# Kernel optimization log

Hardware: AMD Instinct MI355X
Metric: run time of the kernel (lower is better)

Reference implementation:

```python
import jax, jax.numpy as jnp
import numpy as np

B = 131072
IN, H1, H2, OUT = 784, 128, 64, 10


def setup_inputs() -> dict:
    key = jax.random.key(0)
    ks = jax.random.split(key, 10)
    f16 = jnp.float16
    x = jax.random.normal(ks[0], (B, IN), dtype=f16)
    # int4 quantized weights: values in [-8, 7], stored as int32
    w1_q = jax.random.randint(ks[1], (H1, IN), -8, 8, dtype=jnp.int32)
    w2_q = jax.random.randint(ks[2], (H2, H1), -8, 8, dtype=jnp.int32)
    w3_q = jax.random.randint(ks[3], (OUT, H2), -8, 8, dtype=jnp.int32)
    # per-output-channel scales ~ kaiming-ish magnitude / 7 (int4 max)
    s1 = (jax.random.uniform(ks[4], (H1,), dtype=f16) * f16(0.02) + f16(0.005))
    s2 = (jax.random.uniform(ks[5], (H2,), dtype=f16) * f16(0.02) + f16(0.005))
    s3 = (jax.random.uniform(ks[6], (OUT,), dtype=f16) * f16(0.02) + f16(0.005))
    b1 = jax.random.normal(ks[7], (H1,), dtype=f16) * f16(0.01)
    b2 = jax.random.normal(ks[8], (H2,), dtype=f16) * f16(0.01)
    b3 = jax.random.normal(ks[9], (OUT,), dtype=f16) * f16(0.01)
    return {"x": x, "w1_q": w1_q, "s1": s1, "b1": b1,
            "w2_q": w2_q, "s2": s2, "b2": b2,
            "w3_q": w3_q, "s3": s3, "b3": b3}


def _qlinear(x, w_q, scale, bias):
    # W4A16: dequantize int4 weights with per-out-channel scale, fp16 GEMM + bias
    w = w_q.astype(jnp.float16) * scale[:, None]  # [out, in]
    return jnp.dot(x, w.T) + bias


def reference(x, w1_q, s1, b1, w2_q, s2, b2, w3_q, s3, b3):
    x = x.reshape(-1, IN)
    h = jax.nn.relu(_qlinear(x, w1_q, s1, b1))
    h = jax.nn.relu(_qlinear(h, w2_q, s2, b2))
    return _qlinear(h, w3_q, s3, b3)
```

## Files before the change

kernel.cpp:

```cpp
#include <hip/hip_runtime.h>
#include <hip/hip_bf16.h>

#define NROWS 131072
#define KIN   784
#define H1N   128
#define H2N   64
#define OUTN  10

#define W1P_DW    12800
#define W2C_ELEMS (16 * 64 * 8)
#define W3_ELEMS  (16 * 64)

typedef short s16x8 __attribute__((ext_vector_type(8)));
typedef float f32x4 __attribute__((ext_vector_type(4)));
typedef __hip_bfloat16 bf16;

static __device__ __forceinline__ short b2s(float f) {
    bf16 h = __float2bfloat16(f);
    return *reinterpret_cast<short*>(&h);
}
static __device__ __forceinline__ s16x8 cvt8(f32x4 a, f32x4 b) {
    s16x8 r;
    r[0] = b2s(a[0]); r[1] = b2s(a[1]); r[2] = b2s(a[2]); r[3] = b2s(a[3]);
    r[4] = b2s(b[0]); r[5] = b2s(b[1]); r[6] = b2s(b[2]); r[7] = b2s(b[3]);
    return r;
}
static __device__ __forceinline__ s16x8 unpack8(unsigned d) {
    s16x8 r;
#pragma unroll
    for (int j = 0; j < 8; ++j) {
        int v = ((int)(d << (28 - 4 * j))) >> 28;
        r[j] = b2s((float)v);
    }
    return r;
}
static __device__ __forceinline__ void gl2lds16(const void* g, char* l) {
    __builtin_amdgcn_global_load_lds(
        (const __attribute__((address_space(1))) void*)g,
        (__attribute__((address_space(3))) void*)l, 16, 0, 0);
}
static __device__ __forceinline__ void gl2lds4(const void* g, char* l) {
    __builtin_amdgcn_global_load_lds(
        (const __attribute__((address_space(1))) void*)g,
        (__attribute__((address_space(3))) void*)l, 4, 0, 0);
}

#define WAITV(N) do { asm volatile("s_waitcnt vmcnt(" #N ")" ::: "memory"); \
                      __builtin_amdgcn_sched_barrier(0); } while (0)
#define WAITL()  do { asm volatile("s_waitcnt lgkmcnt(0)" ::: "memory"); \
                      __builtin_amdgcn_sched_barrier(0); } while (0)
#define BAR()    __builtin_amdgcn_s_barrier()

__global__ __launch_bounds__(256) void dequant_kernel(
    const int* __restrict__ w1q, const float* __restrict__ s1,
    const int* __restrict__ w2q, const float* __restrict__ s2,
    const int* __restrict__ w3q, const float* __restrict__ s3,
    unsigned* __restrict__ w1p, bf16* __restrict__ w2c, bf16* __restrict__ w3d)
{
    const int total = W1P_DW + W2C_ELEMS + W3_ELEMS;
    for (int i = blockIdx.x * blockDim.x + threadIdx.x; i < total;
         i += gridDim.x * blockDim.x) {
        if (i < W1P_DW) {
            int kb = i >> 9, rem = i & 511;
            int kg = rem >> 7, col_s = rem & 127;
            int col = (col_s - 8 * kg) & 127;
            unsigned d = 0;
#pragma unroll
            for (int j = 0; j < 8; ++j) {
                int k = kb * 32 + kg * 8 + j;
                unsigned q = 0;
                if (k < KIN) q = (unsigned)w1q[col * KIN + k] & 0xFu;
                d |= q << (4 * j);
            }
            w1p[i] = d;
        } else if (i < W1P_DW + W2C_ELEMS) {
            int t = i - W1P_DW;
            int kb = t >> 9, rem = t & 511;
            int col = rem >> 3, j = rem & 7;
            int k = kb * 8 + j;
            w2c[t] = __float2bfloat16((float)w2q[col * H1N + k] * s2[col]);
        } else {
            int t = i - W1P_DW - W2C_ELEMS;
            int r = t >> 6, c = t & 63;
            float v = 0.0f;
            if (r < OUTN) v = (float)w3q[r * H2N + c] * s3[r];
            w3d[t] = __float2bfloat16(v);
        }
    }
}

__global__ __launch_bounds__(256, 5) void mlp_kernel(
    const float* __restrict__ x,
    const unsigned* __restrict__ w1p,
    const bf16*  __restrict__ w2c,
    const bf16*  __restrict__ w3d,
    const float* __restrict__ s1,
    const float* __restrict__ b1,
    const float* __restrict__ b2,
    const float* __restrict__ b3,
    float* __restrict__ out)
{
    __shared__ __align__(16) char lds[30720];

    const int tid  = threadIdx.x;
    const int lane = tid & 63;
    const int wv   = tid >> 6;
    const int r16  = lane & 15;
    const int kg   = lane >> 4;
    const int kgo  = kg * 8;
    const int rg   = wv >> 1;
    const int cg   = wv & 1;

    const int i3 = lane >> 3;
    const int i7 = lane & 7;
    const int sw = i7 ^ i3;
    const int adj = (sw >= 4) ? 16 : 0;

    const long long rowBlk = (long long)blockIdx.x * 64;
    const float* gA0 = x + (rowBlk + wv * 16 + i3) * (long long)KIN + sw * 4;
    const float* gA1 = gA0 + 8LL * KIN;
    const unsigned* gBp = w1p + wv * 128 + lane;

    const int aoff = (rg * 32 + r16) * 128 + (((2 * kg) ^ (r16 & 7)) * 16);
    const int bcol = cg * 64 + r16 + 8 * kg;

#define STAGE(W, S) do {                                                      \
        char* ad_ = lds + (S) * 8192 + wv * 2048;                             \
        char* bd_ = lds + 24576 + (S) * 2048 + wv * 512;                      \
        if ((W) < 24) {                                                       \
            gl2lds16(gA0 + (W) * 32, ad_);                                    \
            gl2lds16(gA1 + (W) * 32, ad_ + 1024);                             \
            gl2lds4(gBp + (W) * 512, bd_);                                    \
            gl2lds4(gBp + (W) * 512 + 64, bd_ + 256);                         \
        } else {                       \
            gl2lds16(gA0 + 768 - adj, ad_);                                   \
            gl2lds16(gA1 + 768 - adj, ad_ + 1024);                            \
            gl2lds4(gBp + 24 * 512, bd_);                                     \
            gl2lds4(gBp + 24 * 512 + 64, bd_ + 256);                          \
        }                                                                     \
    } while (0)

    STAGE(0, 0);
    STAGE(1, 1);
    STAGE(2, 2);

    f32x4 acc1[2][4];
#pragma unroll
    for (int i = 0; i < 2; ++i)
#pragma unroll
        for (int j = 0; j < 4; ++j) acc1[i][j] = (f32x4){0.f, 0.f, 0.f, 0.f};

    int sc = 0;
#pragma unroll 1
    for (int t = 0; t < 23; ++t) {
        WAITV(8);
        BAR();
        const char* sa = lds + sc * 8192;
        f32x4 q00 = *(const f32x4*)(sa + aoff);
        f32x4 q01 = *(const f32x4*)(sa + (aoff ^ 16));
        f32x4 q10 = *(const f32x4*)(sa + aoff + 2048);
        f32x4 q11 = *(const f32x4*)(sa + (aoff ^ 16) + 2048);
        const char* sb = lds + 24576 + sc * 2048 + kg * 512;
        unsigned bw4[4];
#pragma unroll
        for (int nj = 0; nj < 4; ++nj)
            bw4[nj] = *(const unsigned*)(sb + (((bcol + nj * 16) & 127) << 2));
        WAITL();
        BAR();
        if (t <= 21) STAGE(t + 3, sc);
        s16x8 a0 = cvt8(q00, q01);
        s16x8 a1 = cvt8(q10, q11);
#pragma unroll
        for (int nj = 0; nj < 4; ++nj) {
            s16x8 bf = unpack8(bw4[nj]);
            acc1[0][nj] = __builtin_amdgcn_mfma_f32_16x16x32_bf16(a0, bf, acc1[0][nj], 0, 0, 0);
            acc1[1][nj] = __builtin_amdgcn_mfma_f32_16x16x32_bf16(a1, bf, acc1[1][nj], 0, 0, 0);
        }
        sc = (sc == 2) ? 0 : sc + 1;
    }
    {
        WAITV(4);
        BAR();
        const char* sa = lds + sc * 8192;
        f32x4 q00 = *(const f32x4*)(sa + aoff);
        f32x4 q01 = *(const f32x4*)(sa + (aoff ^ 16));
        f32x4 q10 = *(const f32x4*)(sa + aoff + 2048);
        f32x4 q11 = *(const f32x4*)(sa + (aoff ^ 16) + 2048);
        const char* sb = lds + 24576 + sc * 2048 + kg * 512;
        unsigned bw4[4];
#pragma unroll
        for (int nj = 0; nj < 4; ++nj)
            bw4[nj] = *(const unsigned*)(sb + (((bcol + nj * 16) & 127) << 2));
        WAITL();
        BAR();
        s16x8 a0 = cvt8(q00, q01);
        s16x8 a1 = cvt8(q10, q11);
#pragma unroll
        for (int nj = 0; nj < 4; ++nj) {
            s16x8 bf = unpack8(bw4[nj]);
            acc1[0][nj] = __builtin_amdgcn_mfma_f32_16x16x32_bf16(a0, bf, acc1[0][nj], 0, 0, 0);
            acc1[1][nj] = __builtin_amdgcn_mfma_f32_16x16x32_bf16(a1, bf, acc1[1][nj], 0, 0, 0);
        }
        sc = (sc == 2) ? 0 : sc + 1;
    }
    {
        WAITV(0);
        BAR();
        const char* sa = lds + sc * 8192;
        f32x4 q00 = *(const f32x4*)(sa + aoff);
        f32x4 q01 = *(const f32x4*)(sa + (aoff ^ 16));
        f32x4 q10 = *(const f32x4*)(sa + aoff + 2048);
        f32x4 q11 = *(const f32x4*)(sa + (aoff ^ 16) + 2048);
        const char* sb = lds + 24576 + sc * 2048 + kg * 512;
        unsigned bw4[4];
#pragma unroll
        for (int nj = 0; nj < 4; ++nj)
            bw4[nj] = *(const unsigned*)(sb + (((bcol + nj * 16) & 127) << 2));
        WAITL();
        BAR();
        s16x8 a0 = cvt8(q00, q01);
        s16x8 a1 = cvt8(q10, q11);
#pragma unroll
        for (int nj = 0; nj < 4; ++nj) {
            s16x8 bf = unpack8(bw4[nj]);
            acc1[0][nj] = __builtin_amdgcn_mfma_f32_16x16x32_bf16(a0, bf, acc1[0][nj], 0, 0, 0);
            acc1[1][nj] = __builtin_amdgcn_mfma_f32_16x16x32_bf16(a1, bf, acc1[1][nj], 0, 0, 0);
        }
    }
#undef STAGE

    short* h1s = (short*)lds;
#pragma unroll
    for (int nj = 0; nj < 4; ++nj) {
        const int col = cg * 64 + nj * 16 + r16;
        const float sc1 = s1[col];
        const float bb = b1[col];
#pragma unroll
        for (int mi = 0; mi < 2; ++mi)
#pragma unroll
            for (int r = 0; r < 4; ++r) {
                const int row = rg * 32 + mi * 16 + kg * 4 + r;
                h1s[row * 132 + col] = b2s(fmaxf(acc1[mi][nj][r] * sc1 + bb, 0.0f));
            }
    }
    __syncthreads();

    f32x4 acc2[4];
#pragma unroll
    for (int j = 0; j < 4; ++j) acc2[j] = (f32x4){0.f, 0.f, 0.f, 0.f};

#pragma unroll
    for (int it = 0; it < 4; ++it) {
        const int kk = it * 32 + kgo;
        s16x8 a = *(const s16x8*)(h1s + (wv * 16 + r16) * 132 + kk);
        const bf16* bp2 = w2c + (size_t)(it * 4 + kg) * 512 + (size_t)r16 * 8;
#pragma unroll
        for (int nj = 0; nj < 4; ++nj) {
            s16x8 b = *(const s16x8*)(bp2 + nj * 128);
            acc2[nj] = __builtin_amdgcn_mfma_f32_16x16x32_bf16(a, b, acc2[nj], 0, 0, 0);
        }
    }

    short* h2s = (short*)(lds + 16896);
#pragma unroll
    for (int nj = 0; nj < 4; ++nj) {
        const int col = nj * 16 + r16;
        const float bb = b2[col];
#pragma unroll
        for (int r = 0; r < 4; ++r)
            h2s[(wv * 16 + kg * 4 + r) * 68 + col] = b2s(fmaxf(acc2[nj][r] + bb, 0.0f));
    }

    f32x4 acc3 = (f32x4){0.f, 0.f, 0.f, 0.f};
#pragma unroll
    for (int it = 0; it < 2; ++it) {
        const int kk = it * 32 + kgo;
        s16x8 a = *(const s16x8*)(h2s + (wv * 16 + r16) * 68 + kk);
        s16x8 b = *(const s16x8*)(w3d + r16 * H2N + kk);
        acc3 = __builtin_amdgcn_mfma_f32_16x16x32_bf16(a, b, acc3, 0, 0, 0);
    }

    float* ob = (float*)(lds + (wv * 16) * 264);
    const float bb3 = (r16 < OUTN) ? b3[r16] : 0.0f;
#pragma unroll
    for (int r = 0; r < 4; ++r) {
        const int row = kg * 4 + r;
        if (r16 < OUTN) ob[row * OUTN + r16] = acc3[r] + bb3;
    }
    const long long obase = (rowBlk + wv * 16) * OUTN;
    for (int i = lane; i < 16 * OUTN; i += 64) out[obase + i] = ob[i];
}

extern "C" void kernel_launch(void* const* d_in, const int* in_sizes, int n_in,
                              void* d_out, int out_size, void* d_ws, size_t ws_size,
                              hipStream_t stream) {
    const float* x   = (const float*)d_in[0];
    const int*   w1q = (const int*)d_in[1];
    const float* s1  = (const float*)d_in[2];
    const float* b1  = (const float*)d_in[3];
    const int*   w2q = (const int*)d_in[4];
    const float* s2  = (const float*)d_in[5];
    const float* b2  = (const float*)d_in[6];
    const int*   w3q = (const int*)d_in[7];
    const float* s3  = (const float*)d_in[8];
    const float* b3  = (const float*)d_in[9];
    float* out = (float*)d_out;

    unsigned* w1p = (unsigned*)d_ws;
    bf16* w2c = (bf16*)(w1p + W1P_DW);
    bf16* w3d = w2c + W2C_ELEMS;

    dequant_kernel<<<128, 256, 0, stream>>>(w1q, s1, w2q, s2, w3q, s3, w1p, w2c, w3d);
    mlp_kernel<<<NROWS / 64, 256, 0, stream>>>(x, w1p, w2c, w3d, s1, b1, b2, b3, out);
}
```

Baseline: 95.41 us.

## Switch layer-1 pipeline from triple to double buffering for higher occupancy

Reduces the staged global-to-LDS pipeline for the first GEMM from three stages to two, shrinking shared memory from 30720 to 25600 bytes and raising the launch-bounds occupancy hint from 5 to 6 blocks. The loop now ping-pongs on t&1 with a prefetch distance of two and waits with a smaller outstanding-load count. More resident blocks should hide memory latency across blocks, at the cost of less in-block prefetch depth and more exposed load latency per iteration. The later epilogue still has to fit its buffers in the smaller LDS allocation.

Result: slower. 111.7 us (+17.1%).

```diff
diff --git a/kernel.cpp b/kernel.cpp
--- a/kernel.cpp
+++ b/kernel.cpp
@@ -89,7 +89,7 @@
     }
 }
 
-__global__ __launch_bounds__(256, 5) void mlp_kernel(
+__global__ __launch_bounds__(256, 6) void mlp_kernel(
     const float* __restrict__ x,
     const unsigned* __restrict__ w1p,
     const bf16*  __restrict__ w2c,
@@ -100,7 +100,7 @@
     const float* __restrict__ b3,
     float* __restrict__ out)
 {
-    __shared__ __align__(16) char lds[30720];
+    __shared__ __align__(16) char lds[25600];
 
     const int tid  = threadIdx.x;
     const int lane = tid & 63;
@@ -126,7 +126,7 @@
 
 #define STAGE(W, S) do {                                                      \
         char* ad_ = lds + (S) * 8192 + wv * 2048;                             \
-        char* bd_ = lds + 24576 + (S) * 2048 + wv * 512;                      \
+        char* bd_ = lds + 16384 + (S) * 2048 + wv * 512;                      \
         if ((W) < 24) {                                                       \
             gl2lds16(gA0 + (W) * 32, ad_);                                    \
             gl2lds16(gA1 + (W) * 32, ad_ + 1024);                             \
@@ -142,7 +142,6 @@
 
     STAGE(0, 0);
     STAGE(1, 1);
-    STAGE(2, 2);
 
     f32x4 acc1[2][4];
 #pragma unroll
@@ -150,24 +149,23 @@
 #pragma unroll
         for (int j = 0; j < 4; ++j) acc1[i][j] = (f32x4){0.f, 0.f, 0.f, 0.f};
 
-    int sc = 0;
 #pragma unroll 1
-    for (int t = 0; t < 23; ++t) {
-        WAITV(8);
-        BAR();
-        const char* sa = lds + sc * 8192;
+    for (int t = 0; t < 24; ++t) {
+        WAITV(4);
+        BAR();
+        const char* sa = lds + (t & 1) * 8192;
         f32x4 q00 = *(const f32x4*)(sa + aoff);
         f32x4 q01 = *(const f32x4*)(sa + (aoff ^ 16));
         f32x4 q10 = *(const f32x4*)(sa + aoff + 2048);
         f32x4 q11 = *(const f32x4*)(sa + (aoff ^ 16) + 2048);
-        const char* sb = lds + 24576 + sc * 2048 + kg * 512;
+        const char* sb = lds + 16384 + (t & 1) * 2048 + kg * 512;
         unsigned bw4[4];
 #pragma unroll
         for (int nj = 0; nj < 4; ++nj)
             bw4[nj] = *(const unsigned*)(sb + (((bcol + nj * 16) & 127) << 2));
         WAITL();
         BAR();
-        if (t <= 21) STAGE(t + 3, sc);
+        if (t < 23) STAGE(t + 2, (t & 1));
         s16x8 a0 = cvt8(q00, q01);
         s16x8 a1 = cvt8(q10, q11);
 #pragma unroll
@@ -176,42 +174,16 @@
             acc1[0][nj] = __builtin_amdgcn_mfma_f32_16x16x32_bf16(a0, bf, acc1[0][nj], 0, 0, 0);
             acc1[1][nj] = __builtin_amdgcn_mfma_f32_16x16x32_bf16(a1, bf, acc1[1][nj], 0, 0, 0);
         }
-        sc = (sc == 2) ? 0 : sc + 1;
     }
     {
-        WAITV(4);
-        BAR();
-        const char* sa = lds + sc * 8192;
+        WAITV(0);
+        BAR();
+        const char* sa = lds + (24 & 1) * 8192;
         f32x4 q00 = *(const f32x4*)(sa + aoff);
         f32x4 q01 = *(const f32x4*)(sa + (aoff ^ 16));
         f32x4 q10 = *(const f32x4*)(sa + aoff + 2048);
         f32x4 q11 = *(const f32x4*)(sa + (aoff ^ 16) + 2048);
-        const char* sb = lds + 24576 + sc * 2048 + kg * 512;
-        unsigned bw4[4];
-#pragma unroll
-        for (int nj = 0; nj < 4; ++nj)
-            bw4[nj] = *(const unsigned*)(sb + (((bcol + nj * 16) & 127) << 2));
-        WAITL();
-        BAR();
-        s16x8 a0 = cvt8(q00, q01);
-        s16x8 a1 = cvt8(q10, q11);
-#pragma unroll
-        for (int nj = 0; nj < 4; ++nj) {
-            s16x8 bf = unpack8(bw4[nj]);
-            acc1[0][nj] = __builtin_amdgcn_mfma_f32_16x16x32_bf16(a0, bf, acc1[0][nj], 0, 0, 0);
-            acc1[1][nj] = __builtin_amdgcn_mfma_f32_16x16x32_bf16(a1, bf, acc1[1][nj], 0, 0, 0);
-        }
-        sc = (sc == 2) ? 0 : sc + 1;
-    }
-    {
-        WAITV(0);
-        BAR();
-        const char* sa = lds + sc * 8192;
-        f32x4 q00 = *(const f32x4*)(sa + aoff);
-        f32x4 q01 = *(const f32x4*)(sa + (aoff ^ 16));
-        f32x4 q10 = *(const f32x4*)(sa + aoff + 2048);
-        f32x4 q11 = *(const f32x4*)(sa + (aoff ^ 16) + 2048);
-        const char* sb = lds + 24576 + sc * 2048 + kg * 512;
+        const char* sb = lds + 16384 + (24 & 1) * 2048 + kg * 512;
         unsigned bw4[4];
 #pragma unroll
         for (int nj = 0; nj < 4; ++nj)
```
